# Optimization experiments

Hardware: AMD Instinct MI355X
Metric: run time of the kernel (lower is better)

Reference implementation:

```python
import jax, jax.numpy as jnp
import numpy as np

D_MODEL = 1024
D_INTERNAL = 256


def setup_inputs() -> dict:
    key = jax.random.key(0)
    ks = jax.random.split(key, 12)
    s = 0.02
    return {
        "x": jax.random.normal(ks[0], (4, 2048, D_MODEL), dtype=jnp.float32),
        "Wq": jax.random.normal(ks[1], (D_MODEL, D_INTERNAL), dtype=jnp.float32) * s,
        "bq": jnp.zeros((D_INTERNAL,), dtype=jnp.float32),
        "Wk": jax.random.normal(ks[2], (D_MODEL, D_INTERNAL), dtype=jnp.float32) * s,
        "bk": jnp.zeros((D_INTERNAL,), dtype=jnp.float32),
        "Wv": jax.random.normal(ks[3], (D_MODEL, D_MODEL), dtype=jnp.float32) * s,
        "bv": jnp.zeros((D_MODEL,), dtype=jnp.float32),
        "W1": jax.random.normal(ks[4], (D_MODEL, D_MODEL), dtype=jnp.float32) * s,
        "b1": jnp.zeros((D_MODEL,), dtype=jnp.float32),
        "W2": jax.random.normal(ks[5], (D_MODEL, D_MODEL), dtype=jnp.float32) * s,
        "b2": jnp.zeros((D_MODEL,), dtype=jnp.float32),
    }


def reference(x, Wq, bq, Wk, bk, Wv, bv, W1, b1, W2, b2):
    # x: [B, S, D]
    S = x.shape[-2]
    q = x @ Wq + bq            # [B, S, Di]
    k = x @ Wk + bk            # [B, S, Di]
    v = x @ Wv + bv            # [B, S, D]
    scale = 1.0 / jnp.sqrt(jnp.asarray(q.shape[-1], dtype=x.dtype))
    scores = jnp.einsum('bqd,bkd->bqk', q, k) * scale  # [B, S, S]
    causal_mask = jnp.triu(jnp.ones((S, S), dtype=bool), k=1)
    scores = jnp.where(causal_mask, -jnp.inf, scores)
    attn = jax.nn.softmax(scores, axis=-1)             # [B, S, S]
    attention = jnp.einsum('bqk,bkd->bqd', attn, v)    # [B, S, D]
    h = x + attention
    ff = jax.nn.relu(h @ W1 + b1) @ W2 + b2
    return h + ff, attn
```

## Files before the change

kernel.cpp:

```cpp
#include <hip/hip_runtime.h>
#include <hip/hip_bf16.h>

#define BM 128
#define BN 128

typedef __bf16 bf16x8 __attribute__((ext_vector_type(8)));
typedef float f32x4 __attribute__((ext_vector_type(4)));
typedef unsigned short u16;

__device__ __forceinline__ u16 f2bf(float f) {
    __bf16 b = (__bf16)f;
    return __builtin_bit_cast(u16, b);
}
__device__ __forceinline__ float bf2f(u16 u) {
    __bf16 b = __builtin_bit_cast(__bf16, u);
    return (float)b;
}

__device__ __forceinline__ void gload_lds16(const void* g, void* l) {
    __builtin_amdgcn_global_load_lds(
        (const __attribute__((address_space(1))) void*)g,
        (__attribute__((address_space(3))) void*)l,
        16, 0, 0);
}

template <int MODE>
__global__ __launch_bounds__(256)
void gemm_bt(const u16* __restrict__ A, int lda, long long a_bs,
             const u16* __restrict__ Bt, int ldb, long long b_bs,
             int Kdim, int ldc, long long c_bs,
             const float* __restrict__ bias, float scale,
             const void* __restrict__ resid, long long r_bs,
             void* __restrict__ out, int causal)
{
    int bx = blockIdx.x, by = blockIdx.y, bz = blockIdx.z;
    if (causal == 3) {
        const int t = blockIdx.x;
        int byy = (int)((sqrtf(8.f * (float)t + 1.f) - 1.f) * 0.5f);
        while ((byy + 1) * (byy + 2) / 2 <= t) byy++;
        while (byy * (byy + 1) / 2 > t) byy--;
        by = byy; bx = t - byy * (byy + 1) / 2; bz = blockIdx.y;
    }
    if (causal == 2 && bz >= 2) by = (int)gridDim.y - 1 - by;
    const int kend = (causal == 2) ? min(Kdim, (by + 1) * BM) : Kdim;

    A  += (long long)bz * a_bs;
    Bt += (long long)bz * b_bs;

    const int m0 = by * BM, n0 = bx * BN;
    const int tid = threadIdx.x;
    const int wave = tid >> 6, lane = tid & 63;
    const int wy = wave >> 1, wx = wave & 1;
    const int lr = lane >> 2, lc8 = (lane & 3) * 8;
    const int lane15 = lane & 15, kq = lane >> 4;

    __shared__ __align__(16) u16 As[2][BM * 32];
    __shared__ __align__(16) u16 Bs[2][BN * 32];

    f32x4 acc[4][4] = {};

    for (int k0 = 0; k0 < kend; k0 += 64) {
        __syncthreads();
        #pragma unroll
        for (int h = 0; h < 2; h++) {
            const int kh = k0 + h * 32 + lc8;
            #pragma unroll
            for (int it = 0; it < 2; it++) {
                const int row = wave * 16 + it * 64 + lr;
                gload_lds16(A  + (size_t)(m0 + row) * lda + kh,
                            &As[h][(wave * 16 + it * 64) * 32]);
                gload_lds16(Bt + (size_t)(n0 + row) * ldb + kh,
                            &Bs[h][(wave * 16 + it * 64) * 32]);
            }
        }
        __syncthreads();

        #pragma unroll
        for (int h = 0; h < 2; h++) {
            bf16x8 av[4], bv[4];
            #pragma unroll
            for (int i = 0; i < 4; i++)
                av[i] = *(const bf16x8*)&As[h][(wy * 64 + i * 16 + lane15) * 32 + kq * 8];
            #pragma unroll
            for (int j = 0; j < 4; j++)
                bv[j] = *(const bf16x8*)&Bs[h][(wx * 64 + j * 16 + lane15) * 32 + kq * 8];
            #pragma unroll
            for (int i = 0; i < 4; i++)
                #pragma unroll
                for (int j = 0; j < 4; j++)
                    acc[i][j] = __builtin_amdgcn_mfma_f32_16x16x32_bf16(av[i], bv[j], acc[i][j], 0, 0, 0);
        }
    }

    if (MODE == 6 && n0 >= 512) {
        u16* o = (u16*)resid;
        #pragma unroll
        for (int i = 0; i < 4; i++) {
            const int r = m0 + wy * 64 + i * 16 + kq * 4;
            const size_t base = (size_t)(r >> 11) * 1024 * 2048 + (r & 2047);
            #pragma unroll
            for (int j = 0; j < 4; j++) {
                const int c = n0 + wx * 64 + j * 16 + lane15;
                const float bj = bias[c];
                ushort4 pk;
                pk.x = f2bf(acc[i][j][0] + bj);
                pk.y = f2bf(acc[i][j][1] + bj);
                pk.z = f2bf(acc[i][j][2] + bj);
                pk.w = f2bf(acc[i][j][3] + bj);
                *(ushort4*)&o[base + (size_t)(c - 512) * 2048] = pk;
            }
        }
    } else {
        #pragma unroll
        for (int i = 0; i < 4; i++) {
            const int rl = m0 + wy * 64 + i * 16 + kq * 4;
            #pragma unroll
            for (int j = 0; j < 4; j++) {
                const int c = n0 + wx * 64 + j * 16 + lane15;
                float bj = 0.f;
                if (MODE == 4 || MODE == 5 || MODE == 6) bj = bias[c];
                #pragma unroll
                for (int rg = 0; rg < 4; rg++) {
                    const int r = rl + rg;
                    const size_t idx = (size_t)bz * c_bs + (size_t)r * ldc + c;
                    const float v = acc[i][j][rg];
                    if (MODE == 2) {
                        float p = __expf(v * scale);
                        if (c > r) p = 0.f;
                        ((u16*)out)[idx] = f2bf(p);
                    } else if (MODE == 3) {
                        const u16* xr = (const u16*)resid;
                        const float linv = bias[(size_t)bz * 2048 + r];
                        const float h = bf2f(xr[(size_t)bz * r_bs + (size_t)r * ldc + c]) + v * linv;
                        ((u16*)out)[idx] = f2bf(h);
                    } else if (MODE == 4) {
                        ((u16*)out)[idx] = f2bf(fmaxf(v + bj, 0.f));
                    } else if (MODE == 5) {
                        const u16* hb = (const u16*)resid;
                        ((float*)out)[idx] = v + bj + bf2f(hb[(size_t)r * ldc + c]);
                    } else if (MODE == 6) {
                        ((u16*)out)[idx] = f2bf(v + bj);
                    }
                }
            }
        }
    }
}

__global__ __launch_bounds__(256)
void prep_x(const float* __restrict__ x, u16* __restrict__ xb)
{
    const int N4 = 8388608 / 4;
    for (int i = blockIdx.x * blockDim.x + threadIdx.x; i < N4; i += gridDim.x * blockDim.x) {
        const float4 v = ((const float4*)x)[i];
        ushort4 o;
        o.x = f2bf(v.x); o.y = f2bf(v.y); o.z = f2bf(v.z); o.w = f2bf(v.w);
        ((ushort4*)xb)[i] = o;
    }
}

__global__ __launch_bounds__(256)
void prep_w(const float* __restrict__ Wq, const float* __restrict__ bq,
            const float* __restrict__ Wk, const float* __restrict__ bk,
            const float* __restrict__ Wv, const float* __restrict__ bv,
            const float* __restrict__ b1, const float* __restrict__ b2,
            const float* __restrict__ W1, const float* __restrict__ W2,
            u16* __restrict__ WqkT, u16* __restrict__ WvT,
            u16* __restrict__ W1T, u16* __restrict__ W2T, float* __restrict__ biasv)
{
    const int bid = blockIdx.x, tid = threadIdx.x;
    if (bid == 896) {
        for (int t = tid; t < 3584; t += 256) {
            if (t < 512)       biasv[t] = (t < 256) ? bq[t] : bk[t - 256];
            else if (t < 1536) biasv[t] = bv[t - 512];
            else if (t < 2560) biasv[t] = b1[t - 1536];
            else               biasv[t] = b2[t - 2560];
        }
        return;
    }
    const float* src; u16* dst; int ld_src, kt, nt, nbase;
    if (bid < 128) {
        const int job = bid >> 6, t = bid & 63;
        src = job ? Wk : Wq; ld_src = 256;
        kt = t >> 2; nt = t & 3; nbase = job * 256 + nt * 64;
        dst = WqkT;
    } else {
        const int j = bid - 128, w = j >> 8, t = j & 255;
        src = (w == 0) ? Wv : (w == 1) ? W1 : W2; ld_src = 1024;
        kt = t >> 4; nt = t & 15; nbase = nt * 64;
        dst = (w == 0) ? WvT : (w == 1) ? W1T : W2T;
    }
    const int k0 = kt * 64, n0 = (nbase & 255) | (nbase & ~255 & 0);
    const int n0s = (ld_src == 256) ? (nbase & 255) : nbase;

    __shared__ float tile[64][65];
    const int ri = tid >> 4, j4 = (tid & 15) * 4;
    #pragma unroll
    for (int rr = 0; rr < 4; rr++) {
        const int i = ri + rr * 16;
        const float4 v = *(const float4*)&src[(size_t)(k0 + i) * ld_src + n0s + j4];
        tile[j4 + 0][i] = v.x;
        tile[j4 + 1][i] = v.y;
        tile[j4 + 2][i] = v.z;
        tile[j4 + 3][i] = v.w;
    }
    __syncthreads();
    const int n = tid >> 2, ks = (tid & 3) * 16;
    ushort4 o[4];
    #pragma unroll
    for (int c = 0; c < 4; c++) {
        o[c].x = f2bf(tile[n][ks + c * 4 + 0]);
        o[c].y = f2bf(tile[n][ks + c * 4 + 1]);
        o[c].z = f2bf(tile[n][ks + c * 4 + 2]);
        o[c].w = f2bf(tile[n][ks + c * 4 + 3]);
    }
    u16* drow = &dst[(size_t)(nbase + n) * 1024 + k0 + ks];
    #pragma unroll
    for (int c = 0; c < 4; c++) *(ushort4*)&drow[c * 4] = o[c];
}

__device__ __forceinline__ float wave_sum(float v) {
    #pragma unroll
    for (int off = 32; off > 0; off >>= 1) v += __shfl_xor(v, off, 64);
    return v;
}

__global__ __launch_bounds__(256)
void norm_kernel(const u16* __restrict__ attnb, float* __restrict__ attn,
                 float* __restrict__ linv)
{
    const int S = 2048;
    const int row = blockIdx.x;
    const int q = row & (S - 1);
    const int kpad = (q + 128) & ~127;
    const u16* brow = attnb + (size_t)row * S;
    float* srow = attn + (size_t)row * S;
    __shared__ float red[4];
    const int tid = threadIdx.x, wv = tid >> 6, ln = tid & 63;
    const int k = tid * 8;

    float vals[8];
    float lsum = 0.f;
    if (k < kpad) {
        const ushort4 a = *(const ushort4*)&brow[k];
        const ushort4 b = *(const ushort4*)&brow[k + 4];
        vals[0] = bf2f(a.x); vals[1] = bf2f(a.y); vals[2] = bf2f(a.z); vals[3] = bf2f(a.w);
        vals[4] = bf2f(b.x); vals[5] = bf2f(b.y); vals[6] = bf2f(b.z); vals[7] = bf2f(b.w);
        #pragma unroll
        for (int c = 0; c < 8; c++) lsum += vals[c];
    }
    lsum = wave_sum(lsum);
    if (ln == 0) red[wv] = lsum;
    __syncthreads();
    const float rinv = 1.f / (red[0] + red[1] + red[2] + red[3]);

    float4 o0 = {0.f, 0.f, 0.f, 0.f}, o1 = {0.f, 0.f, 0.f, 0.f};
    if (k < kpad) {
        o0 = make_float4(vals[0] * rinv, vals[1] * rinv, vals[2] * rinv, vals[3] * rinv);
        o1 = make_float4(vals[4] * rinv, vals[5] * rinv, vals[6] * rinv, vals[7] * rinv);
    }
    *(float4*)&srow[k] = o0;
    *(float4*)&srow[k + 4] = o1;
    if (tid == 0) linv[row] = rinv;
}

extern "C" void kernel_launch(void* const* d_in, const int* in_sizes, int n_in,
                              void* d_out, int out_size, void* d_ws, size_t ws_size,
                              hipStream_t stream)
{
    const float* x  = (const float*)d_in[0];
    const float* Wq = (const float*)d_in[1];
    const float* bq = (const float*)d_in[2];
    const float* Wk = (const float*)d_in[3];
    const float* bk = (const float*)d_in[4];
    const float* Wv = (const float*)d_in[5];
    const float* bv = (const float*)d_in[6];
    const float* W1 = (const float*)d_in[7];
    const float* b1 = (const float*)d_in[8];
    const float* W2 = (const float*)d_in[9];
    const float* b2 = (const float*)d_in[10];

    const int B = 4, S = 2048, D = 1024, BS = B * S;

    char* ws = (char*)d_ws;
    u16*   xb    = (u16*)(ws + 0);
    u16*   WqkT  = (u16*)(ws + 16777216);
    u16*   WvT   = (u16*)(ws + 17825792);
    u16*   W1T   = (u16*)(ws + 19922944);
    u16*   W2T   = (u16*)(ws + 22020096);
    float* biasv = (float*)(ws + 24117248);
    u16*   QK    = (u16*)(ws + 24133632);
    u16*   Vt    = (u16*)(ws + 32522240);
    u16*   attnb = (u16*)(ws + 49299456);
    float* linv  = (float*)(ws + 83886080);
    u16*   hb    = xb;
    u16*   ff1   = attnb;

    float* out0 = (float*)d_out;
    float* attn = out0 + (size_t)BS * D;

    const dim3 blk(256);

    prep_x<<<dim3(1024), blk, 0, stream>>>(x, xb);
    prep_w<<<dim3(897), blk, 0, stream>>>(Wq, bq, Wk, bk, Wv, bv, b1, b2, W1, W2,
                                          WqkT, WvT, W1T, W2T, biasv);

    gemm_bt<6><<<dim3(12, 64, 1), blk, 0, stream>>>(
        xb, 1024, 0, WqkT, 1024, 0, 1024, 512, 0,
        biasv, 1.f, Vt, 0, QK, 0);

    gemm_bt<2><<<dim3(136, 4, 1), blk, 0, stream>>>(
        QK, 512, (long long)S * 512, QK + 256, 512, (long long)S * 512,
        256, S, (long long)S * S, nullptr, 0.0625f, nullptr, 0, attnb, 3);

    norm_kernel<<<dim3(BS), blk, 0, stream>>>(attnb, attn, linv);

    gemm_bt<3><<<dim3(8, 16, 4), blk, 0, stream>>>(
        attnb, S, (long long)S * S, Vt, S, (long long)D * S,
        S, D, (long long)S * D, linv, 1.f, xb, (long long)S * D, hb, 2);

    gemm_bt<4><<<dim3(8, 64, 1), blk, 0, stream>>>(
        hb, 1024, 0, W1T, 1024, 0, 1024, 1024, 0,
        biasv + 1536, 1.f, nullptr, 0, ff1, 0);

    gemm_bt<5><<<dim3(8, 64, 1), blk, 0, stream>>>(
        ff1, 1024, 0, W2T, 1024, 0, 1024, 1024, 0,
        biasv + 2560, 1.f, hb, 0, out0, 0);
}
```

Measured before the change: 330.8 us.

## Add triple-buffered 256x128 GEMM kernel with swizzled LDS for projection and FFN

Adds a new gemm_bt2 kernel with 512 threads, 256x128 output tiles, a three-stage LDS ring filled by direct global-to-LDS loads with partial vmcnt waits, an XOR-swizzled LDS layout, and s_setprio around the MFMA blocks. It is used for the fused QKV projection and both FFN GEMMs, while the old kernel keeps only the attention modes. The goal is to hide global load latency behind MFMA work and reduce LDS bank conflicts. The cost is much more LDS per block, which lowers occupancy, and fewer blocks in the grid.

```diff
diff --git a/kernel.cpp b/kernel.cpp
--- a/kernel.cpp
+++ b/kernel.cpp
@@ -92,15 +92,114 @@
         }
     }
 
+    #pragma unroll
+    for (int i = 0; i < 4; i++) {
+        const int rl = m0 + wy * 64 + i * 16 + kq * 4;
+        #pragma unroll
+        for (int j = 0; j < 4; j++) {
+            const int c = n0 + wx * 64 + j * 16 + lane15;
+            #pragma unroll
+            for (int rg = 0; rg < 4; rg++) {
+                const int r = rl + rg;
+                const size_t idx = (size_t)bz * c_bs + (size_t)r * ldc + c;
+                const float v = acc[i][j][rg];
+                if (MODE == 2) {
+                    float p = __expf(v * scale);
+                    if (c > r) p = 0.f;
+                    ((u16*)out)[idx] = f2bf(p);
+                } else if (MODE == 3) {
+                    const u16* xr = (const u16*)resid;
+                    const float linv = bias[(size_t)bz * 2048 + r];
+                    const float h = bf2f(xr[(size_t)bz * r_bs + (size_t)r * ldc + c]) + v * linv;
+                    ((u16*)out)[idx] = f2bf(h);
+                }
+            }
+        }
+    }
+}
+
+template <int MODE>
+__global__ __launch_bounds__(512, 2)
+void gemm_bt2(const u16* __restrict__ A, int lda,
+              const u16* __restrict__ Bt, int ldb,
+              int Kdim, int ldc,
+              const float* __restrict__ bias,
+              const void* __restrict__ resid,
+              void* __restrict__ out)
+{
+    const int m0 = blockIdx.y * 256, n0 = blockIdx.x * 128;
+    const int tid = threadIdx.x;
+    const int wave = tid >> 6, lane = tid & 63;
+    const int wr = wave >> 1, wc = wave & 1;
+    const int lane15 = lane & 15, kq = lane >> 4;
+    const int lr = lane >> 2;
+    const int swzc8 = ((lane & 3) ^ ((lane >> 3) & 3)) * 8;
+    const int lslot = lane15 * 32 + ((kq ^ ((lane15 >> 1) & 3)) * 8);
+
+    __shared__ __align__(16) u16 As[3][2][256 * 32];
+    __shared__ __align__(16) u16 Bs[3][2][128 * 32];
+
+    f32x4 acc[4][4] = {};
+    const int NT = Kdim >> 6;
+
+    auto stage = [&](int buf, int t) {
+        const int k0 = t << 6;
+        #pragma unroll
+        for (int h = 0; h < 2; h++) {
+            const int kh = k0 + h * 32 + swzc8;
+            #pragma unroll
+            for (int it = 0; it < 2; it++) {
+                const int row = wave * 16 + it * 128 + lr;
+                gload_lds16(A + (size_t)(m0 + row) * lda + kh,
+                            &As[buf][h][(wave * 16 + it * 128) * 32]);
+            }
+            gload_lds16(Bt + (size_t)(n0 + wave * 16 + lr) * ldb + kh,
+                        &Bs[buf][h][(wave * 16) * 32]);
+        }
+    };
+
+    stage(0, 0);
+    stage(1, 1);
+
+    int cur = 0;
+    for (int t = 0; t < NT; t++) {
+        if (t < NT - 1) asm volatile("s_waitcnt vmcnt(6) lgkmcnt(0)" ::: "memory");
+        else            asm volatile("s_waitcnt vmcnt(0) lgkmcnt(0)" ::: "memory");
+        __builtin_amdgcn_s_barrier();
+        if (t + 2 < NT) {
+            int tgt = cur + 2; if (tgt >= 3) tgt -= 3;
+            stage(tgt, t + 2);
+        }
+
+        #pragma unroll
+        for (int h = 0; h < 2; h++) {
+            bf16x8 av[4], bv[4];
+            #pragma unroll
+            for (int i = 0; i < 4; i++)
+                av[i] = *(const bf16x8*)&As[cur][h][(wr * 4 + i) * 512 + lslot];
+            #pragma unroll
+            for (int j = 0; j < 4; j++)
+                bv[j] = *(const bf16x8*)&Bs[cur][h][(wc * 4 + j) * 512 + lslot];
+            __builtin_amdgcn_s_setprio(1);
+            #pragma unroll
+            for (int i = 0; i < 4; i++)
+                #pragma unroll
+                for (int j = 0; j < 4; j++)
+                    acc[i][j] = __builtin_amdgcn_mfma_f32_16x16x32_bf16(av[i], bv[j], acc[i][j], 0, 0, 0);
+            __builtin_amdgcn_s_setprio(0);
+        }
+        cur++; if (cur == 3) cur = 0;
+    }
+
     if (MODE == 6 && n0 >= 512) {
         u16* o = (u16*)resid;
         #pragma unroll
         for (int i = 0; i < 4; i++) {
-            const int r = m0 + wy * 64 + i * 16 + kq * 4;
+            const int r = m0 + wr * 64 + i * 16 + kq * 4;
             const size_t base = (size_t)(r >> 11) * 1024 * 2048 + (r & 2047);
             #pragma unroll
             for (int j = 0; j < 4; j++) {
-                const int c = n0 + wx * 64 + j * 16 + lane15;
+                const int c = n0 + wc * 64 + j * 16 + lane15;
                 const float bj = bias[c];
                 ushort4 pk;
                 pk.x = f2bf(acc[i][j][0] + bj);
@@ -113,31 +212,21 @@
     } else {
         #pragma unroll
         for (int i = 0; i < 4; i++) {
-            const int rl = m0 + wy * 64 + i * 16 + kq * 4;
+            const int rl = m0 + wr * 64 + i * 16 + kq * 4;
             #pragma unroll
             for (int j = 0; j < 4; j++) {
-                const int c = n0 + wx * 64 + j * 16 + lane15;
-                float bj = 0.f;
-                if (MODE == 4 || MODE == 5 || MODE == 6) bj = bias[c];
+                const int c = n0 + wc * 64 + j * 16 + lane15;
+                const float bj = bias[c];
                 #pragma unroll
                 for (int rg = 0; rg < 4; rg++) {
                     const int r = rl + rg;
-                    const size_t idx = (size_t)bz * c_bs + (size_t)r * ldc + c;
+                    const size_t idx = (size_t)r * ldc + c;
                     const float v = acc[i][j][rg];
-                    if (MODE == 2) {
-                        float p = __expf(v * scale);
-                        if (c > r) p = 0.f;
-                        ((u16*)out)[idx] = f2bf(p);
-                    } else if (MODE == 3) {
-                        const u16* xr = (const u16*)resid;
-                        const float linv = bias[(size_t)bz * 2048 + r];
-                        const float h = bf2f(xr[(size_t)bz * r_bs + (size_t)r * ldc + c]) + v * linv;
-                        ((u16*)out)[idx] = f2bf(h);
-                    } else if (MODE == 4) {
+                    if (MODE == 4) {
                         ((u16*)out)[idx] = f2bf(fmaxf(v + bj, 0.f));
                     } else if (MODE == 5) {
                         const u16* hb = (const u16*)resid;
-                        ((float*)out)[idx] = v + bj + bf2f(hb[(size_t)r * ldc + c]);
+                        ((float*)out)[idx] = v + bj + bf2f(hb[idx]);
                     } else if (MODE == 6) {
                         ((u16*)out)[idx] = f2bf(v + bj);
                     }
@@ -190,7 +279,7 @@
         kt = t >> 4; nt = t & 15; nbase = nt * 64;
         dst = (w == 0) ? WvT : (w == 1) ? W1T : W2T;
     }
-    const int k0 = kt * 64, n0 = (nbase & 255) | (nbase & ~255 & 0);
+    const int k0 = kt * 64;
     const int n0s = (ld_src == 256) ? (nbase & 255) : nbase;
 
     __shared__ float tile[64][65];
@@ -305,9 +394,8 @@
     prep_w<<<dim3(897), blk, 0, stream>>>(Wq, bq, Wk, bk, Wv, bv, b1, b2, W1, W2,
                                           WqkT, WvT, W1T, W2T, biasv);
 
-    gemm_bt<6><<<dim3(12, 64, 1), blk, 0, stream>>>(
-        xb, 1024, 0, WqkT, 1024, 0, 1024, 512, 0,
-        biasv, 1.f, Vt, 0, QK, 0);
+    gemm_bt2<6><<<dim3(12, 32), dim3(512), 0, stream>>>(
+        xb, 1024, WqkT, 1024, 1024, 512, biasv, Vt, QK);
 
     gemm_bt<2><<<dim3(136, 4, 1), blk, 0, stream>>>(
         QK, 512, (long long)S * 512, QK + 256, 512, (long long)S * 512,
@@ -319,11 +407,9 @@
         attnb, S, (long long)S * S, Vt, S, (long long)D * S,
         S, D, (long long)S * D, linv, 1.f, xb, (long long)S * D, hb, 2);
 
-    gemm_bt<4><<<dim3(8, 64, 1), blk, 0, stream>>>(
-        hb, 1024, 0, W1T, 1024, 0, 1024, 1024, 0,
-        biasv + 1536, 1.f, nullptr, 0, ff1, 0);
-
-    gemm_bt<5><<<dim3(8, 64, 1), blk, 0, stream>>>(
-        ff1, 1024, 0, W2T, 1024, 0, 1024, 1024, 0,
-        biasv + 2560, 1.f, hb, 0, out0, 0);
-}
+    gemm_bt2<4><<<dim3(8, 32), dim3(512), 0, stream>>>(
+        hb, 1024, W1T, 1024, 1024, 1024, biasv + 1536, nullptr, ff1);
+
+    gemm_bt2<5><<<dim3(8, 32), dim3(512), 0, stream>>>(
+        ff1, 1024, W2T, 1024, 1024, 1024, biasv + 2560, hb, out0);
+}
```

Measured after the change: 347.5 us. 1.05x slower.
